# Performance work log

Hardware: AMD Instinct MI355X
Metric: run time of the kernel (lower is better)

## Reference

```python
import jax, jax.numpy as jnp
import numpy as np

B = 256
NO_A, NF_A = 64, 4   # class A: n_obj, n_field (all state fields)
NO_B, NF_B = 32, 3   # class B
NS = NF_A + NF_B     # total state fields = 7
DIN, DL, DG, DH = 128, 64, 64, 256
DGE = DG * NF_A + DG * NF_B          # 448 global encoding dim
DIN_A = DGE + DL * NF_A              # 704 decoder input dim, class A
DIN_B = DGE + DL * NF_B              # 640 decoder input dim, class B
NP = 2  # distribution params per field (mean, scale)


def lrelu(x):
    return jnp.where(x >= 0, x, 0.01 * x)


def setup_inputs() -> dict:
    key = jax.random.key(0)
    ks = iter(jax.random.split(key, 40))
    def rn(shape, s=1.0):
        return jax.random.normal(next(ks), shape, jnp.float32) * s
    def w(shape):
        return rn(shape, 0.05)
    def rb(shape):
        return jax.random.randint(next(ks), shape, 0, 2).astype(bool)
    inp = dict(
        x_A=rn((B, NO_A, NF_A, DIN)),
        x_B=rn((B, NO_B, NF_B, DIN)),
        global_mask=rb((B, NS, NF_A + NF_B)),
        local_mask_A=rb((B, NF_A, NF_A)),
        local_mask_B=rb((B, NF_B, NF_B)),
        objmask_A=rb((B, NO_A)),
        objmask_B=rb((B, NO_B)),
        enc_Wl_A=w((DIN, DL)), enc_bl_A=w((DL,)),
        enc_Wg_A=w((DIN, DG)), enc_bg_A=w((DG,)),
        enc_Wl_B=w((DIN, DL)), enc_bl_B=w((DL,)),
        enc_Wg_B=w((DIN, DG)), enc_bg_B=w((DG,)),
        dec_W1_A=w((NF_A, DIN_A, DH)), dec_b1_A=w((NF_A, DH)),
        dec_W2_A=w((NF_A, DH, DH)), dec_b2_A=w((NF_A, DH)),
        dec_Wp_A=w((NF_A, DH, NP)), dec_bp_A=w((NF_A, NP)),
        dec_W1_B=w((NF_B, DIN_B, DH)), dec_b1_B=w((NF_B, DH)),
        dec_W2_B=w((NF_B, DH, DH)), dec_b2_B=w((NF_B, DH)),
        dec_Wp_B=w((NF_B, DH, NP)), dec_bp_B=w((NF_B, NP)),
        rw_W1=w((DGE, DH)), rw_b1=w((DH,)),
        rw_W2=w((DH, DH)), rw_b2=w((DH,)),
        rw_W3=w((DH, 1)), rw_b3=w((1,)),
    )
    return inp


def encode_local(x, Wl, bl, attrmask):
    # x: (B, O, F, DIN) -> (B, O, S, F*DL), masked_retain over attrmask (B, S, F)
    h = jax.nn.relu(x @ Wl + bl)                                  # (B,O,F,DL)
    y = jnp.where(attrmask[:, None, :, :, None], h[:, :, None, :, :], 0.0)  # (B,O,S,F,DL)
    return y.reshape(y.shape[0], y.shape[1], y.shape[2], -1)


def encode_global(x, Wg, bg, attrmask, objmask):
    # x: (B, O, F, DIN), attrmask: (B, NS, F), objmask: (B, O)
    h = x @ Wg + bg                                               # (B,O,F,DG)
    h = jnp.where(objmask[:, :, None, None], h, 0.0)
    r = jax.nn.relu(jnp.sum(h, axis=1))                           # (B,F,DG) sum-pool over objects
    y = jnp.where(attrmask[:, :, :, None], r[:, None], 0.0)       # (B,NS,F,DG)
    y = jnp.concatenate([y, r[:, None]], axis=1)                  # (B,NS+1,F,DG)
    return y.reshape(y.shape[0], y.shape[1], -1)


def decode(x, W1, b1, W2, b2, Wp, bp):
    # x: (B, O, S, Din); per-field (s) decoders stacked on leading axis
    h = lrelu(jnp.einsum('bosi,sid->bosd', x, W1) + b1)
    h = lrelu(jnp.einsum('bosd,sde->bose', h, W2) + b2)
    return jnp.einsum('bose,sep->bosp', h, Wp) + bp               # (B,O,S,NP)


def reference(x_A, x_B, global_mask, local_mask_A, local_mask_B, objmask_A, objmask_B,
              enc_Wl_A, enc_bl_A, enc_Wg_A, enc_bg_A,
              enc_Wl_B, enc_bl_B, enc_Wg_B, enc_bg_B,
              dec_W1_A, dec_b1_A, dec_W2_A, dec_b2_A, dec_Wp_A, dec_bp_A,
              dec_W1_B, dec_b1_B, dec_W2_B, dec_b2_B, dec_Wp_B, dec_bp_B,
              rw_W1, rw_b1, rw_W2, rw_b2, rw_W3, rw_b3):
    g_A = encode_global(x_A, enc_Wg_A, enc_bg_A, global_mask[:, :, :NF_A], objmask_A)
    g_B = encode_global(x_B, enc_Wg_B, enc_bg_B, global_mask[:, :, NF_A:], objmask_B)
    G = jnp.concatenate([g_A, g_B], axis=2)                       # (B, NS+1, DGE)

    l_A = encode_local(x_A, enc_Wl_A, enc_bl_A, local_mask_A)     # (B,NO_A,NF_A,NF_A*DL)
    gs_A = jnp.broadcast_to(G[:, None, :NF_A, :], (B, NO_A, NF_A, DGE))
    out_A = decode(jnp.concatenate([l_A, gs_A], axis=3),
                   dec_W1_A, dec_b1_A, dec_W2_A, dec_b2_A, dec_Wp_A, dec_bp_A)

    l_B = encode_local(x_B, enc_Wl_B, enc_bl_B, local_mask_B)
    gs_B = jnp.broadcast_to(G[:, None, NF_A:NS, :], (B, NO_B, NF_B, DGE))
    out_B = decode(jnp.concatenate([l_B, gs_B], axis=3),
                   dec_W1_B, dec_b1_B, dec_W2_B, dec_b2_B, dec_Wp_B, dec_bp_B)

    h = lrelu(G[:, -1, :] @ rw_W1 + rw_b1)
    h = lrelu(h @ rw_W2 + rw_b2)
    reward = (h @ rw_W3 + rw_b3)[:, 0]                            # (B,)
    return out_A, out_B, reward
```

## Files before the change

kernel.cpp:

```cpp
#include <hip/hip_runtime.h>
#include <hip/hip_bf16.h>

constexpr int Bn   = 256;
constexpr int NOA  = 64, NFA = 4;
constexpr int NOB  = 32, NFB = 3;
constexpr int NS   = 7;
constexpr int DIN  = 128, DL = 64, DG = 64, DH = 256;
constexpr int DGE  = 448;
constexpr int DINA = 704;
constexpr int DINB = 640;

typedef short  short8v __attribute__((ext_vector_type(8)));
typedef float  f32x4   __attribute__((ext_vector_type(4)));

__device__ __forceinline__ unsigned short f2bf(float x) {
  union { float f; unsigned int u; } a; a.f = x;
  unsigned int r = a.u + 0x7fff + ((a.u >> 16) & 1);
  return (unsigned short)(r >> 16);
}


struct MidArgs {
  const float *xA, *xB, *WlA, *WlB, *blA, *blB;
  unsigned short *hlA, *hlB;
  const int *omA, *omB;
  const float *WgA, *bgA, *WgB, *bgB;
  float *rA, *rB;
  const float *W1A, *W1B, *W2A, *W2B;
  unsigned short *W1tA, *W1tB, *W1gtA, *W1gtB, *W2tA, *W2tB;
};

template<int F>
__device__ void hl_body(const float* __restrict__ x, const float* __restrict__ Wl,
                        const float* __restrict__ bl, unsigned short* __restrict__ hlf,
                        int m0, unsigned char* smem) {
  auto Asb = reinterpret_cast<unsigned short(*)[72]>(smem);
  auto Bsb = reinterpret_cast<unsigned short(*)[136]>(smem + 36864);
  float (*tile)[65] = reinterpret_cast<float(*)[65]>(smem);
  const int t = threadIdx.x, w = t >> 6, lane = t & 63;
  const int lr = lane & 15, lg = lane >> 4;
  constexpr int KB1 = 2 * F;

#pragma unroll
  for (int i = 0; i < 32; ++i) {
    int idx = t + i * 256;
    tile[idx >> 6][idx & 63] = Wl[idx];
  }
  __syncthreads();
#pragma unroll
  for (int i = 0; i < 32; ++i) {
    int idx = t + i * 256;
    int n = idx >> 7, k = idx & 127;
    Bsb[n][k] = f2bf(tile[k][n]);
  }
  __syncthreads();

  f32x4 acc[4][4] = {};
  for (int k0 = 0; k0 < DIN; k0 += 64) {
    const float* xp = x + (size_t)(m0 + t) * DIN + k0;
#pragma unroll
    for (int j = 0; j < 8; ++j) {
      float4 a = *(const float4*)(xp + j * 8);
      float4 b = *(const float4*)(xp + j * 8 + 4);
      union { short8v v; unsigned short e[8]; } u;
      u.e[0] = f2bf(a.x); u.e[1] = f2bf(a.y); u.e[2] = f2bf(a.z); u.e[3] = f2bf(a.w);
      u.e[4] = f2bf(b.x); u.e[5] = f2bf(b.y); u.e[6] = f2bf(b.z); u.e[7] = f2bf(b.w);
      *reinterpret_cast<short8v*>(&Asb[t][j * 8]) = u.v;
    }
#pragma unroll
    for (int ks = 0; ks < 2; ++ks) {
      short8v af[4], bf[4];
#pragma unroll
      for (int mi = 0; mi < 4; ++mi)
        af[mi] = *reinterpret_cast<const short8v*>(&Asb[w * 64 + mi * 16 + lr][ks * 32 + lg * 8]);
#pragma unroll
      for (int ni = 0; ni < 4; ++ni)
        bf[ni] = *reinterpret_cast<const short8v*>(&Bsb[ni * 16 + lr][k0 + ks * 32 + lg * 8]);
#pragma unroll
      for (int mi = 0; mi < 4; ++mi)
#pragma unroll
        for (int ni = 0; ni < 4; ++ni)
          acc[mi][ni] = __builtin_amdgcn_mfma_f32_16x16x32_bf16(
              af[mi], bf[ni], acc[mi][ni], 0, 0, 0);
    }
  }
#pragma unroll
  for (int mi = 0; mi < 4; ++mi)
#pragma unroll
    for (int ni = 0; ni < 4; ++ni)
#pragma unroll
      for (int reg = 0; reg < 4; ++reg) {
        int row = mi * 16 + lg * 4 + reg;
        int col = ni * 16 + lr;
        float v = fmaxf(acc[mi][ni][reg] + bl[col], 0.f);
        Asb[w * 64 + row][col] = f2bf(v);
      }
  const int mpb = m0 + w * 64;
#pragma unroll
  for (int j = 0; j < 8; ++j) {
    int c = lane + j * 64;
    int ml = c >> 3, dls = c & 7;
    int mp = mpb + ml;
    int mrow = mp / F, f = mp % F;
    int m6 = mrow >> 6, mi = (mrow >> 4) & 3, lr2 = mrow & 15;
    int kb = 2 * f + (dls >> 2), lg2 = dls & 3;
    size_t dst = ((((size_t)m6 * KB1 + kb) * 4 + mi) * 64 + (lg2 * 16 + lr2)) * 8;
    *reinterpret_cast<short8v*>(hlf + dst) =
        *reinterpret_cast<const short8v*>(&Asb[w * 64 + ml][dls * 8]);
  }
}

template<int O, int F>
__device__ void xsum_rg_body(const float* __restrict__ x, const int* __restrict__ om,
                             const float* __restrict__ Wg, const float* __restrict__ bg,
                             float* __restrict__ r, int b, unsigned char* smem) {
  float* xsm = reinterpret_cast<float*>(smem + 36864 + 17408);
  const int t = threadIdx.x, f = t >> 6, lane = t & 63;
  if (f >= F) return;
  unsigned long long bal = __ballot(lane < O && om[(size_t)b * O + lane] != 0);
  float cnt = (float)__popcll(bal);
  float a0 = 0.f, a1 = 0.f;
  const float* xb = x + ((size_t)b * O * F + f) * DIN + lane;
#pragma unroll 8
  for (int o = 0; o < O; ++o) {
    float m = (float)((bal >> o) & 1ull);
    a0 += m * xb[(size_t)o * F * DIN];
    a1 += m * xb[(size_t)o * F * DIN + 64];
  }
  xsm[f * 128 + lane] = a0;
  xsm[f * 128 + lane + 64] = a1;
  asm volatile("s_waitcnt lgkmcnt(0)" ::: "memory");
  float acc = 0.f;
  const float* wp = Wg + lane;
#pragma unroll 8
  for (int i = 0; i < DIN; ++i) acc += xsm[f * 128 + i] * wp[(size_t)i * DG];
  acc += cnt * bg[lane];
  r[((size_t)b * F + f) * DG + lane] = fmaxf(acc, 0.f);
}

__device__ void wtrans_tile(const float* __restrict__ src, unsigned short* __restrict__ dst,
                            int N, int DINc, int koff, int Kout,
                            int s, int kt, int nt, unsigned char* smem) {
  float (*tile)[65] = reinterpret_cast<float(*)[65]>(smem);
  const int t = threadIdx.x;
#pragma unroll
  for (int i = 0; i < 16; ++i) {
    int rr = (t >> 6) + i * 4, c = t & 63;
    tile[rr][c] = src[((size_t)s * DINc + koff + kt * 64 + rr) * N + nt * 64 + c];
  }
  __syncthreads();
#pragma unroll
  for (int i = 0; i < 2; ++i) {
    int cidx = t + i * 256;
    int n = cidx >> 3, kc = (cidx & 7) * 8;
    union { short8v v; unsigned short e[8]; } u;
#pragma unroll
    for (int j = 0; j < 8; ++j) u.e[j] = f2bf(tile[kc + j][n]);
    *reinterpret_cast<short8v*>(dst + ((size_t)s * N + nt * 64 + n) * Kout + kt * 64 + kc) = u.v;
  }
}

__device__ void wtrans_frag(const float* __restrict__ src, unsigned short* __restrict__ dst,
                            int DINc, int koff, int KB,
                            int s, int kt, int nt, unsigned char* smem) {
  float (*tile)[65] = reinterpret_cast<float(*)[65]>(smem);
  const int t = threadIdx.x;
#pragma unroll
  for (int i = 0; i < 16; ++i) {
    int rr = (t >> 6) + i * 4, c = t & 63;
    tile[rr][c] = src[((size_t)s * DINc + koff + kt * 64 + rr) * 256 + nt * 64 + c];
  }
  __syncthreads();
#pragma unroll
  for (int i = 0; i < 2; ++i) {
    int cidx = t + i * 256;
    int nl = cidx >> 3, kslot = cidx & 7;
    union { short8v v; unsigned short e[8]; } u;
#pragma unroll
    for (int j = 0; j < 8; ++j) u.e[j] = f2bf(tile[kslot * 8 + j][nl]);
    int kb = kt * 2 + (kslot >> 2);
    int lane = (kslot & 3) * 16 + (nl & 15);
    int nchunk = nt * 4 + (nl >> 4);
    *reinterpret_cast<short8v*>(
        dst + ((((size_t)s * KB + kb) * 16 + nchunk) * 64 + lane) * 8) = u.v;
  }
}

__global__ __launch_bounds__(256) void mid_kernel(MidArgs a) {
  __shared__ __align__(16) unsigned char smem[56320];
  const int bid = blockIdx.x;
  if (bid < 256) {
    hl_body<NFA>(a.xA, a.WlA, a.blA, a.hlA, bid * 256, smem);
    xsum_rg_body<NOA, NFA>(a.xA, a.omA, a.WgA, a.bgA, a.rA, bid, smem);
  } else if (bid < 352) {
    hl_body<NFB>(a.xB, a.WlB, a.blB, a.hlB, (bid - 256) * 256, smem);
  } else if (bid < 608) {
    xsum_rg_body<NOB, NFB>(a.xB, a.omB, a.WgB, a.bgB, a.rB, bid - 352, smem);
  } else {
    int r = bid - 608;
    if (r < 64)       { wtrans_frag(a.W1A, a.W1tA, DINA, 0, 8,
                                    r / 16, (r % 16) >> 2, r & 3, smem); }
    else if (r < 100) { r -= 64;  wtrans_frag(a.W1B, a.W1tB, DINB, 0, 6,
                                    r / 12, (r % 12) >> 2, r & 3, smem); }
    else if (r < 212) { r -= 100; wtrans_tile(a.W1A, a.W1gtA, 256, DINA, NFA * DL, DGE,
                                    r / 28, (r % 28) >> 2, r & 3, smem); }
    else if (r < 296) { r -= 212; wtrans_tile(a.W1B, a.W1gtB, 256, DINB, NFB * DL, DGE,
                                    r / 28, (r % 28) >> 2, r & 3, smem); }
    else if (r < 360) { r -= 296; wtrans_frag(a.W2A, a.W2tA, DH, 0, 8,
                                    r / 16, (r % 16) >> 2, r & 3, smem); }
    else              { r -= 360; wtrans_frag(a.W2B, a.W2tB, DH, 0, 8,
                                    r / 16, (r % 16) >> 2, r & 3, smem); }
  }
}

struct GprArgs {
  const float *rA, *rB; const int *gm;
  const unsigned short *W1gtA, *W1gtB;
  const float *b1A, *b1B;
  float *g1A, *g1B;
  const float *rwW1, *rwb1, *rwW2, *rwb2, *rwW3, *rwb3;
  float *outR;
  const unsigned short *hlA, *hlB;
};

__device__ void warm_body(const unsigned short* __restrict__ p, int n16) {
  const int4* q = reinterpret_cast<const int4*>(p);
  const int t = threadIdx.x;
  for (int i = 0; i < n16; ++i) {
    int4 v = q[t + i * 256];
    asm volatile("" :: "v"(v.x), "v"(v.y), "v"(v.z), "v"(v.w));
  }
}

__device__ void gpart_body(const GprArgs& a, int bx, int sg, unsigned char* smem) {
  auto Asb = reinterpret_cast<unsigned short(*)[72]>(smem);
  auto Bsb = reinterpret_cast<unsigned short(*)[72]>(smem + 9216);
  const int t = threadIdx.x, w = t >> 6, lane = t & 63;
  const int lr = lane & 15, lg = lane >> 4;
  const int m0 = bx * 64;
  const unsigned short* W1gt; const float* b1; float* g1; int S, sl;
  if (sg < NFA) { W1gt = a.W1gtA; b1 = a.b1A; g1 = a.g1A; S = NFA; sl = sg; }
  else          { W1gt = a.W1gtB; b1 = a.b1B; g1 = a.g1B; S = NFB; sl = sg - NFA; }

  f32x4 acc[4][4] = {};
  for (int kt = 0; kt < 7; ++kt) {
    __syncthreads();
    const int f = kt;
    const float* rsrc = (f < NFA) ? (a.rA + (size_t)f * DG) : (a.rB + (size_t)(f - NFA) * DG);
    const int rstride = (f < NFA) ? NFA * DG : NFB * DG;
#pragma unroll
    for (int i = 0; i < 2; ++i) {
      int c = t + i * 256;
      int row = c >> 3, kc = (c & 7) * 8;
      int b = m0 + row;
      float mk = (a.gm[((size_t)b * NS + sg) * NS + f] != 0) ? 1.f : 0.f;
      const float* rp = rsrc + (size_t)b * rstride + kc;
      union { short8v v; unsigned short e[8]; } u;
#pragma unroll
      for (int j = 0; j < 8; ++j) u.e[j] = f2bf(mk * rp[j]);
      *reinterpret_cast<short8v*>(&Asb[row][kc]) = u.v;
    }
#pragma unroll
    for (int i = 0; i < 8; ++i) {
      int c = t + i * 256;
      int n = c >> 3, kc = (c & 7) * 8;
      *reinterpret_cast<short8v*>(&Bsb[n][kc]) = *reinterpret_cast<const short8v*>(
          W1gt + ((size_t)sl * 256 + n) * DGE + kt * 64 + kc);
    }
    __syncthreads();
#pragma unroll
    for (int ks = 0; ks < 2; ++ks) {
      short8v af[4], bf[4];
#pragma unroll
      for (int mi = 0; mi < 4; ++mi)
        af[mi] = *reinterpret_cast<const short8v*>(&Asb[mi * 16 + lr][ks * 32 + lg * 8]);
#pragma unroll
      for (int ni = 0; ni < 4; ++ni)
        bf[ni] = *reinterpret_cast<const short8v*>(&Bsb[w * 64 + ni * 16 + lr][ks * 32 + lg * 8]);
#pragma unroll
      for (int mi = 0; mi < 4; ++mi)
#pragma unroll
        for (int ni = 0; ni < 4; ++ni)
          acc[mi][ni] = __builtin_amdgcn_mfma_f32_16x16x32_bf16(
              af[mi], bf[ni], acc[mi][ni], 0, 0, 0);
    }
  }
#pragma unroll
  for (int mi = 0; mi < 4; ++mi)
#pragma unroll
    for (int reg = 0; reg < 4; ++reg) {
      int b = m0 + mi * 16 + lg * 4 + reg;
#pragma unroll
      for (int ni = 0; ni < 4; ++ni) {
        int col = w * 64 + ni * 16 + lr;
        g1[((size_t)b * S + sl) * DH + col] = acc[mi][ni][reg] + b1[(size_t)sl * DH + col];
      }
    }
}

__device__ void reward_body(const GprArgs& a, int b, unsigned char* smem) {
  float* Gs = reinterpret_cast<float*>(smem);
  float* h1 = Gs + DGE;
  float* red = h1 + DH;
  const int t = threadIdx.x;
  for (int j = t; j < DGE; j += 256)
    Gs[j] = (j < NFA * DG) ? a.rA[((size_t)b * NFA + (j >> 6)) * DG + (j & 63)]
                           : a.rB[((size_t)b * NFB + ((j - NFA * DG) >> 6)) * DG + (j & 63)];
  __syncthreads();
  float acc = a.rwb1[t];
  for (int j = 0; j < DGE; ++j) acc += Gs[j] * a.rwW1[(size_t)j * DH + t];
  h1[t] = (acc >= 0.f) ? acc : 0.01f * acc;
  __syncthreads();
  acc = a.rwb2[t];
  for (int j = 0; j < DH; ++j) acc += h1[j] * a.rwW2[(size_t)j * DH + t];
  acc = (acc >= 0.f) ? acc : 0.01f * acc;
  red[t] = acc * a.rwW3[t];
  __syncthreads();
  for (int off = 128; off > 0; off >>= 1) {
    if (t < off) red[t] += red[t + off];
    __syncthreads();
  }
  if (t == 0) a.outR[b] = red[0] + a.rwb3[0];
}

__global__ __launch_bounds__(256) void gpr_kernel(GprArgs a) {
  __shared__ __align__(16) unsigned char smem[46080];
  const int bid = blockIdx.x;
  if (bid < 256) {
    int xcd = bid & 7, idx = bid >> 3;
    int m6 = (idx >> 1) * 16 + xcd * 2 + (idx & 1);
    warm_body(a.hlA + (size_t)m6 * 16384, 8);
  } else if (bid < 384) {
    int local = bid - 256;
    int xcd = local & 7, idx = local >> 3;
    int m6 = (idx >> 1) * 16 + xcd * 2 + (idx & 1);
    warm_body(a.hlB + (size_t)m6 * 12288, 6);
  } else if (bid < 412) {
    gpart_body(a, (bid - 384) & 3, (bid - 384) >> 2, smem);
  } else {
    reward_body(a, bid - 412, smem);
  }
}

struct DecArgs {
  const unsigned short *hlA, *hlB, *W1tA, *W1tB, *W2tA, *W2tB;
  const int *lmA, *lmB;
  const float *g1A, *g1B, *WpA, *WpB, *b2A, *b2B, *bpA, *bpB;
  float *outA, *outB;
};

template<int NO, int F>
__device__ __forceinline__ void dec_body(
    int mt, int s, unsigned short* h1s , float* red ,
    const unsigned short* __restrict__ hlf, const int* __restrict__ lm,
    const float* __restrict__ g1,
    const unsigned short* __restrict__ W1f, const unsigned short* __restrict__ W2f,
    const float* __restrict__ Wp, const float* __restrict__ b2,
    const float* __restrict__ bp, float* __restrict__ out) {
  constexpr int KB1 = 2 * F;
  const int t = threadIdx.x, w = t >> 6, lane = t & 63;
  const int lr = lane & 15, lg = lane >> 4;
  const int mh = w >> 2, nq = w & 3;
  const int m6 = mt * 2 + mh;
  const int m0 = mt * 128;

  unsigned mkl = 0, mkh = 0;
#pragma unroll
  for (int f = 0; f < F; ++f) {
    if (NO == 64) {
      unsigned bit = (lm[((size_t)m6 * F + s) * F + f] != 0) ? 1u : 0u;
      mkl |= bit << f; mkh |= bit << f;
    } else {
      int b0 = m6 * 2;
      if (lm[((size_t)b0 * F + s) * F + f])       mkl |= 1u << f;
      if (lm[((size_t)(b0 + 1) * F + s) * F + f]) mkh |= 1u << f;
    }
  }
  float g1r[2][4];
#pragma unroll
  for (int ni = 0; ni < 4; ++ni) {
    int col = nq * 64 + ni * 16 + lr;
    if (NO == 64) {
      g1r[0][ni] = g1[((size_t)m6 * F + s) * DH + col];
      g1r[1][ni] = g1r[0][ni];
    } else {
      g1r[0][ni] = g1[((size_t)(m6 * 2) * F + s) * DH + col];
      g1r[1][ni] = g1[((size_t)(m6 * 2 + 1) * F + s) * DH + col];
    }
  }

  f32x4 acc[4][4] = {};
  const short8v zero8 = {0, 0, 0, 0, 0, 0, 0, 0};

  const unsigned short* Afb = hlf + (size_t)m6 * KB1 * 2048 + lane * 8;
  const unsigned short* B1b = W1f + ((size_t)s * KB1 * 16 + nq * 4) * 512 + lane * 8;
#pragma unroll
  for (int kb = 0; kb < KB1; ++kb) {
    const int f = kb >> 1;
    short8v af[4], bf[4];
#pragma unroll
    for (int mi = 0; mi < 4; ++mi)
      af[mi] = *reinterpret_cast<const short8v*>(Afb + (size_t)kb * 2048 + mi * 512);
    const bool bl = (mkl >> f) & 1, bh = (mkh >> f) & 1;
#pragma unroll
    for (int mi = 0; mi < 4; ++mi) {
      const bool ok = (mi < 2) ? bl : bh;
      af[mi] = ok ? af[mi] : zero8;
    }
#pragma unroll
    for (int ni = 0; ni < 4; ++ni)
      bf[ni] = *reinterpret_cast<const short8v*>(B1b + (size_t)kb * 8192 + ni * 512);
#pragma unroll
    for (int mi = 0; mi < 4; ++mi)
#pragma unroll
      for (int ni = 0; ni < 4; ++ni)
        acc[mi][ni] = __builtin_amdgcn_mfma_f32_16x16x32_bf16(
            af[mi], bf[ni], acc[mi][ni], 0, 0, 0);
  }

#pragma unroll
  for (int mi = 0; mi < 4; ++mi) {
    int gi = (NO == 32) ? (mi >> 1) : 0;
#pragma unroll
    for (int reg = 0; reg < 4; ++reg) {
      int row = mh * 64 + mi * 16 + lg * 4 + reg;
#pragma unroll
      for (int ni = 0; ni < 4; ++ni) {
        int col = nq * 64 + ni * 16 + lr;
        float v = acc[mi][ni][reg] + g1r[gi][ni];
        v = (v >= 0.f) ? v : 0.01f * v;
        h1s[row * 264 + col] = f2bf(v);
        acc[mi][ni][reg] = 0.f;
      }
    }
  }
  __syncthreads();

  const unsigned short* B2b = W2f + ((size_t)s * 8 * 16 + nq * 4) * 512 + lane * 8;
#pragma unroll
  for (int kb = 0; kb < 8; ++kb) {
    short8v af[4], bf[4];
#pragma unroll
    for (int mi = 0; mi < 4; ++mi)
      af[mi] = *reinterpret_cast<const short8v*>(
          h1s + (mh * 64 + mi * 16 + lr) * 264 + kb * 32 + lg * 8);
#pragma unroll
    for (int ni = 0; ni < 4; ++ni)
      bf[ni] = *reinterpret_cast<const short8v*>(B2b + (size_t)kb * 8192 + ni * 512);
#pragma unroll
    for (int mi = 0; mi < 4; ++mi)
#pragma unroll
      for (int ni = 0; ni < 4; ++ni)
        acc[mi][ni] = __builtin_amdgcn_mfma_f32_16x16x32_bf16(
            af[mi], bf[ni], acc[mi][ni], 0, 0, 0);
  }

  float part[4][4][2] = {};
  const float* Wps = Wp + (size_t)s * DH * 2;
  const float* b2s = b2 + (size_t)s * DH;
#pragma unroll
  for (int ni = 0; ni < 4; ++ni) {
    int col = nq * 64 + ni * 16 + lr;
    float wp0 = Wps[col * 2 + 0], wp1 = Wps[col * 2 + 1], bb2 = b2s[col];
#pragma unroll
    for (int mi = 0; mi < 4; ++mi)
#pragma unroll
      for (int reg = 0; reg < 4; ++reg) {
        float v = acc[mi][ni][reg] + bb2;
        v = (v >= 0.f) ? v : 0.01f * v;
        part[mi][reg][0] += v * wp0;
        part[mi][reg][1] += v * wp1;
      }
  }
#pragma unroll
  for (int off = 1; off < 16; off <<= 1)
#pragma unroll
    for (int mi = 0; mi < 4; ++mi)
#pragma unroll
      for (int reg = 0; reg < 4; ++reg) {
        part[mi][reg][0] += __shfl_xor(part[mi][reg][0], off, 64);
        part[mi][reg][1] += __shfl_xor(part[mi][reg][1], off, 64);
      }
  if (lr == 0)
#pragma unroll
    for (int mi = 0; mi < 4; ++mi)
#pragma unroll
      for (int reg = 0; reg < 4; ++reg) {
        int rowin = mi * 16 + lg * 4 + reg;
        red[((size_t)w * 64 + rowin) * 2 + 0] = part[mi][reg][0];
        red[((size_t)w * 64 + rowin) * 2 + 1] = part[mi][reg][1];
      }
  __syncthreads();
  if (t < 256) {
    int row = t >> 1, p = t & 1;
    int mhr = row >> 6, rowin = row & 63;
    float sum = 0.f;
#pragma unroll
    for (int q = 0; q < 4; ++q)
      sum += red[((size_t)(mhr * 4 + q) * 64 + rowin) * 2 + p];
    out[((size_t)(m0 + row) * F + s) * 2 + p] = sum + bp[(size_t)s * 2 + p];
  }
}

__global__ __launch_bounds__(512, 4) void dec_kernel(DecArgs a) {
  __shared__ __align__(16) unsigned short h1s[128 * 264];
  __shared__ float red[1024];
  const int bid = blockIdx.x;
  if (bid < 512) {
    dec_body<NOA, NFA>(bid & 127, bid >> 7, h1s, red, a.hlA, a.lmA, a.g1A,
                       a.W1tA, a.W2tA, a.WpA, a.b2A, a.bpA, a.outA);
  } else {
    int r = bid - 512;
    dec_body<NOB, NFB>(r & 63, r >> 6, h1s, red, a.hlB, a.lmB, a.g1B,
                       a.W1tB, a.W2tB, a.WpB, a.b2B, a.bpB, a.outB);
  }
}

extern "C" void kernel_launch(void* const* d_in, const int* in_sizes, int n_in,
                              void* d_out, int out_size, void* d_ws, size_t ws_size,
                              hipStream_t stream) {
  const float* x_A  = (const float*)d_in[0];
  const float* x_B  = (const float*)d_in[1];
  const int*   gm   = (const int*)d_in[2];
  const int*   lmA  = (const int*)d_in[3];
  const int*   lmB  = (const int*)d_in[4];
  const int*   omA  = (const int*)d_in[5];
  const int*   omB  = (const int*)d_in[6];
  const float* Wl_A = (const float*)d_in[7];
  const float* bl_A = (const float*)d_in[8];
  const float* Wg_A = (const float*)d_in[9];
  const float* bg_A = (const float*)d_in[10];
  const float* Wl_B = (const float*)d_in[11];
  const float* bl_B = (const float*)d_in[12];
  const float* Wg_B = (const float*)d_in[13];
  const float* bg_B = (const float*)d_in[14];
  const float* W1_A = (const float*)d_in[15];
  const float* b1_A = (const float*)d_in[16];
  const float* W2_A = (const float*)d_in[17];
  const float* b2_A = (const float*)d_in[18];
  const float* Wp_A = (const float*)d_in[19];
  const float* bp_A = (const float*)d_in[20];
  const float* W1_B = (const float*)d_in[21];
  const float* b1_B = (const float*)d_in[22];
  const float* W2_B = (const float*)d_in[23];
  const float* b2_B = (const float*)d_in[24];
  const float* Wp_B = (const float*)d_in[25];
  const float* bp_B = (const float*)d_in[26];
  const float* rwW1 = (const float*)d_in[27];
  const float* rwb1 = (const float*)d_in[28];
  const float* rwW2 = (const float*)d_in[29];
  const float* rwb2 = (const float*)d_in[30];
  const float* rwW3 = (const float*)d_in[31];
  const float* rwb3 = (const float*)d_in[32];

  float* ws   = (float*)d_ws;
  float* rA   = ws;
  float* rB   = rA + 65536;
  float* g1A  = rB + 49152;
  float* g1B  = g1A + 262144;
  unsigned short* us    = (unsigned short*)(g1B + 196608);
  unsigned short* hlA   = us;
  unsigned short* hlB   = hlA + 4194304;
  unsigned short* W1tA  = hlB + 1572864;
  unsigned short* W1tB  = W1tA + 262144;
  unsigned short* W2tA  = W1tB + 147456;
  unsigned short* W2tB  = W2tA + 262144;
  unsigned short* W1gtA = W2tB + 196608;
  unsigned short* W1gtB = W1gtA + 458752;

  float* outA = (float*)d_out;
  float* outB = outA + 131072;
  float* outR = outA + 180224;

  MidArgs m;
  m.xA = x_A; m.xB = x_B; m.WlA = Wl_A; m.WlB = Wl_B; m.blA = bl_A; m.blB = bl_B;
  m.hlA = hlA; m.hlB = hlB; m.omA = omA; m.omB = omB;
  m.WgA = Wg_A; m.bgA = bg_A; m.WgB = Wg_B; m.bgB = bg_B;
  m.rA = rA; m.rB = rB;
  m.W1A = W1_A; m.W1B = W1_B; m.W2A = W2_A; m.W2B = W2_B;
  m.W1tA = W1tA; m.W1tB = W1tB; m.W1gtA = W1gtA; m.W1gtB = W1gtB;
  m.W2tA = W2tA; m.W2tB = W2tB;

  GprArgs g;
  g.rA = rA; g.rB = rB; g.gm = gm; g.W1gtA = W1gtA; g.W1gtB = W1gtB;
  g.b1A = b1_A; g.b1B = b1_B; g.g1A = g1A; g.g1B = g1B;
  g.rwW1 = rwW1; g.rwb1 = rwb1; g.rwW2 = rwW2; g.rwb2 = rwb2;
  g.rwW3 = rwW3; g.rwb3 = rwb3; g.outR = outR;
  g.hlA = hlA; g.hlB = hlB;

  DecArgs d;
  d.hlA = hlA; d.hlB = hlB; d.W1tA = W1tA; d.W1tB = W1tB;
  d.W2tA = W2tA; d.W2tB = W2tB; d.lmA = lmA; d.lmB = lmB;
  d.g1A = g1A; d.g1B = g1B; d.WpA = Wp_A; d.WpB = Wp_B;
  d.b2A = b2_A; d.b2B = b2_B; d.bpA = bp_A; d.bpB = bp_B;
  d.outA = outA; d.outB = outB;

  mid_kernel<<<1016, 256, 0, stream>>>(m);
  gpr_kernel<<<668, 256, 0, stream>>>(g);
  dec_kernel<<<704, 512, 0, stream>>>(d);
}
```

Before: 94.42 us.

## Drop L2 warm-up blocks and skip loading masked-out decoder A fragments

Removes the 384 gpr_kernel blocks that only read the hl activation buffers to warm the cache before the decoder, shrinking that launch to the gpart and reward blocks. In the decoder's first GEMM, A-fragment loads for masked-off fields are redirected to the already-loaded weight address, so masked tiles no longer fetch activation data from memory. This cuts memory traffic, but the decoder now reads hl cold from L2 or HBM instead of from a cache that was pre-warmed.

```diff
diff --git a/kernel.cpp b/kernel.cpp
--- a/kernel.cpp
+++ b/kernel.cpp
@@ -220,17 +220,7 @@
   float *g1A, *g1B;
   const float *rwW1, *rwb1, *rwW2, *rwb2, *rwW3, *rwb3;
   float *outR;
-  const unsigned short *hlA, *hlB;
 };
-
-__device__ void warm_body(const unsigned short* __restrict__ p, int n16) {
-  const int4* q = reinterpret_cast<const int4*>(p);
-  const int t = threadIdx.x;
-  for (int i = 0; i < n16; ++i) {
-    int4 v = q[t + i * 256];
-    asm volatile("" :: "v"(v.x), "v"(v.y), "v"(v.z), "v"(v.w));
-  }
-}
 
 __device__ void gpart_body(const GprArgs& a, int bx, int sg, unsigned char* smem) {
   auto Asb = reinterpret_cast<unsigned short(*)[72]>(smem);
@@ -326,20 +316,8 @@
 __global__ __launch_bounds__(256) void gpr_kernel(GprArgs a) {
   __shared__ __align__(16) unsigned char smem[46080];
   const int bid = blockIdx.x;
-  if (bid < 256) {
-    int xcd = bid & 7, idx = bid >> 3;
-    int m6 = (idx >> 1) * 16 + xcd * 2 + (idx & 1);
-    warm_body(a.hlA + (size_t)m6 * 16384, 8);
-  } else if (bid < 384) {
-    int local = bid - 256;
-    int xcd = local & 7, idx = local >> 3;
-    int m6 = (idx >> 1) * 16 + xcd * 2 + (idx & 1);
-    warm_body(a.hlB + (size_t)m6 * 12288, 6);
-  } else if (bid < 412) {
-    gpart_body(a, (bid - 384) & 3, (bid - 384) >> 2, smem);
-  } else {
-    reward_body(a, bid - 412, smem);
-  }
+  if (bid < 28) gpart_body(a, bid & 3, bid >> 2, smem);
+  else          reward_body(a, bid - 28, smem);
 }
 
 struct DecArgs {
@@ -397,19 +375,24 @@
 #pragma unroll
   for (int kb = 0; kb < KB1; ++kb) {
     const int f = kb >> 1;
+    const bool okl = (mkl >> f) & 1, okh = (mkh >> f) & 1;
+    const unsigned short* ab = Afb + (size_t)kb * 2048;
+    const unsigned short* bb = B1b + (size_t)kb * 8192;
     short8v af[4], bf[4];
 #pragma unroll
-    for (int mi = 0; mi < 4; ++mi)
-      af[mi] = *reinterpret_cast<const short8v*>(Afb + (size_t)kb * 2048 + mi * 512);
-    const bool bl = (mkl >> f) & 1, bh = (mkh >> f) & 1;
-#pragma unroll
     for (int mi = 0; mi < 4; ++mi) {
-      const bool ok = (mi < 2) ? bl : bh;
+      const bool ok = (mi < 2) ? okl : okh;
+      const unsigned short* p = ok ? (ab + mi * 512) : bb;
+      af[mi] = *reinterpret_cast<const short8v*>(p);
+    }
+#pragma unroll
+    for (int ni = 0; ni < 4; ++ni)
+      bf[ni] = *reinterpret_cast<const short8v*>(bb + ni * 512);
+#pragma unroll
+    for (int mi = 0; mi < 4; ++mi) {
+      const bool ok = (mi < 2) ? okl : okh;
       af[mi] = ok ? af[mi] : zero8;
     }
-#pragma unroll
-    for (int ni = 0; ni < 4; ++ni)
-      bf[ni] = *reinterpret_cast<const short8v*>(B1b + (size_t)kb * 8192 + ni * 512);
 #pragma unroll
     for (int mi = 0; mi < 4; ++mi)
 #pragma unroll
@@ -586,7 +569,6 @@
   g.b1A = b1_A; g.b1B = b1_B; g.g1A = g1A; g.g1B = g1B;
   g.rwW1 = rwW1; g.rwb1 = rwb1; g.rwW2 = rwW2; g.rwb2 = rwb2;
   g.rwW3 = rwW3; g.rwb3 = rwb3; g.outR = outR;
-  g.hlA = hlA; g.hlB = hlB;
 
   DecArgs d;
   d.hlA = hlA; d.hlB = hlB; d.W1tA = W1tA; d.W1tB = W1tB;
@@ -596,6 +578,6 @@
   d.outA = outA; d.outB = outB;
 
   mid_kernel<<<1016, 256, 0, stream>>>(m);
-  gpr_kernel<<<668, 256, 0, stream>>>(g);
+  gpr_kernel<<<284, 256, 0, stream>>>(g);
   dec_kernel<<<704, 512, 0, stream>>>(d);
 }
```

Result: faster. 88.80 us (-6.0%).
